# Optimization experiments

Measured on AMD Instinct MI355X. Metric: run time of the kernel, lower is better.

## Reference

```python
import jax, jax.numpy as jnp
import numpy as np

B, L, D_MODEL = 4, 2048, 1024
D_STATE, D_CONV, EXPAND, HEADDIM = 128, 4, 2, 64
D_INNER = EXPAND * D_MODEL            # 2048
NHEADS = D_INNER // HEADDIM           # 32
CONV_DIM = D_INNER + 2 * D_STATE      # 2304
D_IN_PROJ = 2 * D_INNER + 2 * D_STATE + NHEADS  # 4448
EPS = 1e-5


def _silu(v):
    return v * jax.nn.sigmoid(v)


def setup_inputs() -> dict:
    key = jax.random.key(0)
    ks = jax.random.split(key, 8)
    x = jax.random.normal(ks[0], (B, L, D_MODEL), dtype=jnp.float32)
    ln_w = jnp.ones((D_MODEL,), jnp.float32)
    ln_b = jnp.zeros((D_MODEL,), jnp.float32)
    in_proj_w = jax.random.normal(ks[1], (D_IN_PROJ, D_MODEL), jnp.float32) * 0.02
    conv_w = jax.random.normal(ks[2], (CONV_DIM, D_CONV), jnp.float32) * 0.2
    conv_b = jnp.zeros((CONV_DIM,), jnp.float32)
    # inverse-softplus of dt sampled in [1e-3, 1e-1], matching mamba2 dt init
    dt_bias = jnp.log(jnp.expm1(jax.random.uniform(ks[3], (NHEADS,), minval=0.001, maxval=0.1)))
    # A sampled uniform in [1,16], stored as log (A = -exp(A_log))
    A_log = jnp.log(jax.random.uniform(ks[4], (NHEADS,), minval=1.0, maxval=16.0))
    D = jnp.ones((NHEADS,), jnp.float32)
    rms_w = jnp.ones((D_INNER,), jnp.float32)
    out_proj_w = jax.random.normal(ks[5], (D_MODEL, D_INNER), jnp.float32) * 0.02
    return {"x": x, "ln_w": ln_w, "ln_b": ln_b, "in_proj_w": in_proj_w,
            "conv_w": conv_w, "conv_b": conv_b, "dt_bias": dt_bias,
            "A_log": A_log, "D": D, "rms_w": rms_w, "out_proj_w": out_proj_w}


def reference(x, ln_w, ln_b, in_proj_w, conv_w, conv_b, dt_bias, A_log, D, rms_w, out_proj_w):
    b = x.shape[0]
    # LayerNorm
    mu = x.mean(-1, keepdims=True)
    var = ((x - mu) ** 2).mean(-1, keepdims=True)
    u = (x - mu) * jax.lax.rsqrt(var + EPS) * ln_w + ln_b
    # input projection -> z | xBC | dt
    zxbcdt = jnp.einsum('bld,ed->ble', u, in_proj_w)
    z = zxbcdt[..., :D_INNER]
    xBC = zxbcdt[..., D_INNER:D_INNER + CONV_DIM]
    dt = jax.nn.softplus(zxbcdt[..., -NHEADS:] + dt_bias)  # (b,l,h)
    # causal depthwise conv along time (kernel D_CONV) + silu
    xpad = jnp.pad(xBC, ((0, 0), (D_CONV - 1, 0), (0, 0)))
    conv = conv_b + sum(conv_w[:, k] * xpad[:, k:k + L, :] for k in range(D_CONV))
    xBC = _silu(conv)
    xh = xBC[..., :D_INNER].reshape(b, L, NHEADS, HEADDIM)       # (b,l,h,p)
    Bm = xBC[..., D_INNER:D_INNER + D_STATE]                      # (b,l,n)
    Cm = xBC[..., D_INNER + D_STATE:]                             # (b,l,n)
    A = -jnp.exp(A_log)                                           # (h,)
    dA = jnp.exp(dt * A)                                          # (b,l,h)
    dtx = dt[..., None] * xh                                      # (b,l,h,p)

    def step(h, inp):
        dA_t, dtx_t, B_t, C_t = inp
        h = dA_t[:, :, None, None] * h + dtx_t[..., None] * B_t[:, None, None, :]
        y_t = jnp.einsum('bhpn,bn->bhp', h, C_t)
        return h, y_t

    h0 = jnp.zeros((b, NHEADS, HEADDIM, D_STATE), x.dtype)
    xs = (dA.transpose(1, 0, 2), dtx.transpose(1, 0, 2, 3),
          Bm.transpose(1, 0, 2), Cm.transpose(1, 0, 2))
    _, ys = jax.lax.scan(step, h0, xs)                            # (l,b,h,p)
    y = ys.transpose(1, 0, 2, 3) + D[None, None, :, None] * xh    # skip term
    y = y.reshape(b, L, D_INNER)
    # gated RMSNorm: rmsnorm(y * silu(z)) * weight
    g = y * _silu(z)
    g = g * jax.lax.rsqrt((g * g).mean(-1, keepdims=True) + EPS) * rms_w
    out = jnp.einsum('ble,de->bld', g, out_proj_w)
    # residual; dropout is identity in eval mode
    return out + x
```

## Files before the change

kernel.cpp:

```cpp
#include <hip/hip_runtime.h>
#include <hip/hip_bf16.h>

#define DEV __device__ __forceinline__

typedef unsigned short u16;
typedef unsigned int u32;
typedef float f32x4 __attribute__((ext_vector_type(4)));
typedef short s16x8 __attribute__((ext_vector_type(8)));

static constexpr int Bb = 4, Ll = 2048, DM = 1024, DI = 2048, NH = 32;
static constexpr int CD = 2304;
static constexpr int NP = 4384;
static constexpr int NP_PAD = 4480;
static constexpr int BL = Bb * Ll;
static constexpr int NC = 32;

DEV float u2f(u16 s) { return __uint_as_float(((u32)s) << 16); }
DEV u16 f2bu(float f) {
  __hip_bfloat16 h = __float2bfloat16(f);
  u16 s; __builtin_memcpy(&s, &h, 2); return s;
}
DEV float blo(u32 u) { return __uint_as_float(u << 16); }
DEV float bhi(u32 u) { return __uint_as_float(u & 0xffff0000u); }

DEV int swz64(int r, int k)  { return r * 64  + ((((k >> 3) ^ (r & 7))) << 3) + (k & 7); }

DEV void gl_lds16(const u16* g, u16* l) {
  __builtin_amdgcn_global_load_lds(
      (const __attribute__((address_space(1))) u32*)g,
      (__attribute__((address_space(3))) u32*)l, 16, 0, 0);
}

__global__ __launch_bounds__(256) void prep_kernel(const float* __restrict__ x,
    const float* __restrict__ w, const float* __restrict__ bia, u16* __restrict__ u,
    const float* __restrict__ w1, u16* __restrict__ W1b,
    const float* __restrict__ w2, u16* __restrict__ W2b) {
  __shared__ float rs[4], rs2[4];
  int tid = threadIdx.x;
  if (blockIdx.x < BL) {
    int row = blockIdx.x;
    const float4* xr = (const float4*)(x + (size_t)row * DM);
    float4 v = xr[tid];
    float s = v.x + v.y + v.z + v.w;
    float s2 = v.x*v.x + v.y*v.y + v.z*v.z + v.w*v.w;
    #pragma unroll
    for (int o = 32; o; o >>= 1) { s += __shfl_down(s, o); s2 += __shfl_down(s2, o); }
    int wv = tid >> 6, ln = tid & 63;
    if (ln == 0) { rs[wv] = s; rs2[wv] = s2; }
    __syncthreads();
    s = rs[0] + rs[1] + rs[2] + rs[3];
    s2 = rs2[0] + rs2[1] + rs2[2] + rs2[3];
    float mu = s * (1.f / DM);
    float var = s2 * (1.f / DM) - mu * mu;
    float inv = rsqrtf(var + 1e-5f);
    float4 wv4 = ((const float4*)w)[tid], bv4 = ((const float4*)bia)[tid];
    ushort4 o;
    o.x = f2bu((v.x - mu) * inv * wv4.x + bv4.x);
    o.y = f2bu((v.y - mu) * inv * wv4.y + bv4.y);
    o.z = f2bu((v.z - mu) * inv * wv4.z + bv4.z);
    o.w = f2bu((v.w - mu) * inv * wv4.w + bv4.w);
    ((ushort4*)(u + (size_t)row * DM))[tid] = o;
  } else {
    const int total1 = NP_PAD * 1024;
    int i = (blockIdx.x - BL) * 256 + tid;
    if (i < total1) {
      int r = i >> 10;
      W1b[i] = (r < NP) ? f2bu(w1[i]) : (u16)0;
    } else {
      int j = i - total1;
      if (j < 1024 * 2048) W2b[j] = f2bu(w2[j]);
    }
  }
}

template<int MODE>
__global__ __launch_bounds__(512, 4) void gemm2p(const u16* __restrict__ A,
    const u16* __restrict__ Bw, void* __restrict__ o0, u16* __restrict__ xbc,
    u16* __restrict__ dtraw, const float* __restrict__ resid) {
  constexpr int K = (MODE == 0) ? 1024 : 2048;
  constexpr int NT = K / 32;
  __shared__ u16 SH[24576];
  int tid = threadIdx.x, wid = tid >> 6, lane = tid & 63;
  int fr = lane & 15, fq = lane >> 4;
  int nb = blockIdx.x;
  int xcd = nb & 7, i = nb >> 3;
  int m0 = (xcd * 4 + (i & 3)) * 256;
  int n0 = (i >> 2) * 128;
  int wm = (wid >> 1) * 64, wn = (wid & 1) * 64;
  int ksrcE = (((lane & 3) ^ ((lane >> 3) & 3)) << 3);
  int lr = lane >> 2;

  f32x4 acc[4][4];
  #pragma unroll
  for (int a = 0; a < 4; a++)
    #pragma unroll
    for (int b = 0; b < 4; b++) acc[a][b] = (f32x4){0.f, 0.f, 0.f, 0.f};

  auto STGA = [&](int t, int dstE) {
    #pragma unroll
    for (int h = 0; h < 2; h++) {
      int r0 = h * 128 + wid * 16;
      gl_lds16(A + (size_t)(m0 + r0 + lr) * K + t * 32 + ksrcE, &SH[dstE + r0 * 32]);
    }
  };
  auto STGB = [&](int t, int dstE) {
    int r0 = wid * 16;
    gl_lds16(Bw + (size_t)(n0 + r0 + lr) * K + t * 32 + ksrcE, &SH[dstE + r0 * 32]);
  };

  STGA(0, 0);
  STGB(0, 16384);
  asm volatile("s_waitcnt vmcnt(0)\n\ts_barrier" ::: "memory");
  for (int t = 0; t < NT; t++) {
    int ca = (t & 1) * 8192, cbf = 16384 + (t & 1) * 4096;
    if (t < NT - 1) {
      STGA(t + 1, ((t + 1) & 1) * 8192);
      STGB(t + 1, 16384 + ((t + 1) & 1) * 4096);
      asm volatile("s_waitcnt vmcnt(3)\n\ts_barrier" ::: "memory");
    } else {
      asm volatile("s_waitcnt vmcnt(0)\n\ts_barrier" ::: "memory");
    }
    s16x8 bB[4];
    #pragma unroll
    for (int nf = 0; nf < 4; nf++) {
      int rb = wn + nf * 16 + fr;
      bB[nf] = *(const s16x8*)&SH[cbf + rb * 32 + ((fq ^ ((rb >> 1) & 3)) << 3)];
    }
    __builtin_amdgcn_s_setprio(1);
    #pragma unroll
    for (int mf = 0; mf < 4; mf++) {
      int ra = wm + mf * 16 + fr;
      s16x8 af = *(const s16x8*)&SH[ca + ra * 32 + ((fq ^ ((ra >> 1) & 3)) << 3)];
      #pragma unroll
      for (int nf = 0; nf < 4; nf++)
        acc[mf][nf] = __builtin_amdgcn_mfma_f32_16x16x32_bf16(af, bB[nf], acc[mf][nf], 0, 0, 0);
    }
    __builtin_amdgcn_s_setprio(0);
    asm volatile("s_barrier" ::: "memory");
  }
  if (MODE == 0) {
    u16* zbuf = (u16*)o0;
    #pragma unroll
    for (int mf = 0; mf < 4; mf++) {
      #pragma unroll
      for (int nf = 0; nf < 4; nf++) {
        int col = n0 + wn + nf * 16 + fr;
        #pragma unroll
        for (int r = 0; r < 4; r++) {
          int row = m0 + wm + mf * 16 + fq * 4 + r;
          float v = acc[mf][nf][r];
          if (col < 2048)       zbuf[(size_t)row * 2048 + col] = f2bu(v);
          else if (col < 4352)  xbc[(size_t)row * 2304 + (col - 2048)] = f2bu(v);
          else if (col < 4384)  dtraw[(size_t)row * 32 + (col - 4352)] = f2bu(v);
        }
      }
    }
  } else {
    float* of = (float*)o0;
    #pragma unroll
    for (int mf = 0; mf < 4; mf++) {
      #pragma unroll
      for (int nf = 0; nf < 4; nf++) {
        int col = n0 + wn + nf * 16 + fr;
        #pragma unroll
        for (int r = 0; r < 4; r++) {
          int row = m0 + wm + mf * 16 + fq * 4 + r;
          of[(size_t)row * 1024 + col] = acc[mf][nf][r] + resid[(size_t)row * 1024 + col];
        }
      }
    }
  }
}

__global__ __launch_bounds__(256) void convdt_kernel(const u16* __restrict__ xbc,
    const float* __restrict__ cw, const float* __restrict__ cb, u16* __restrict__ out,
    const u16* __restrict__ dtraw, const float* __restrict__ dtb,
    const float* __restrict__ alog, float* __restrict__ dtv, float* __restrict__ sv) {
  const int CONV_BLOCKS = (BL * (CD / 8)) / 256;
  if (blockIdx.x < CONV_BLOCKS) {
    int i = blockIdx.x * 256 + threadIdx.x;
    int c8 = i % (CD / 8);
    int bl = i / (CD / 8);
    int l = bl & (Ll - 1);
    int c0 = c8 * 8;
    uint4 R[4];
    #pragma unroll
    for (int k = 0; k < 4; k++) {
      int ls = l - 3 + k;
      if (ls >= 0) R[k] = *(const uint4*)(xbc + (size_t)(bl - 3 + k) * CD + c0);
      else         R[k] = (uint4){0u, 0u, 0u, 0u};
    }
    u16 o[8];
    #pragma unroll
    for (int e = 0; e < 8; e++) {
      float acc = cb[c0 + e];
      float4 wv = *(const float4*)(cw + (size_t)(c0 + e) * 4);
      float wk[4] = {wv.x, wv.y, wv.z, wv.w};
      #pragma unroll
      for (int k = 0; k < 4; k++) {
        u32 word = (&R[k].x)[e >> 1];
        float xv = (e & 1) ? bhi(word) : blo(word);
        acc += wk[k] * xv;
      }
      float sg = 1.f / (1.f + __expf(-acc));
      o[e] = f2bu(acc * sg);
    }
    uint4 ov;
    ov.x = (u32)o[0] | ((u32)o[1] << 16);
    ov.y = (u32)o[2] | ((u32)o[3] << 16);
    ov.z = (u32)o[4] | ((u32)o[5] << 16);
    ov.w = (u32)o[6] | ((u32)o[7] << 16);
    *(uint4*)(out + (size_t)bl * CD + c0) = ov;
  } else {
    int wid = threadIdx.x >> 6, lane = threadIdx.x & 63;
    int g = (blockIdx.x - CONV_BLOCKS) * 4 + wid;
    int b = g >> 10, h = (g >> 5) & 31, c = g & 31;
    int t = c * 64 + lane;
    float raw = u2f(dtraw[(size_t)(b * Ll + t) * 32 + h]);
    float v = raw + dtb[h];
    float dt = (v > 20.f) ? v : log1pf(__expf(v));
    float a = -dt * __expf(alog[h]);
    float s = a;
    #pragma unroll
    for (int o = 1; o < 64; o <<= 1) {
      float u = __shfl_up(s, o);
      if (lane >= o) s += u;
    }
    int idx = (b * 32 + h) * Ll + t;
    dtv[idx] = dt;
    sv[idx] = s;
  }
}

__global__ __launch_bounds__(256) void chunk_state(const u16* __restrict__ conv,
    const float* __restrict__ dtv, const float* __restrict__ sv,
    u16* __restrict__ S) {
  __shared__ u16 xsT[64 * 64];
  __shared__ u16 BT[128 * 64];
  int gid = blockIdx.x;
  int h = gid & 31, c = (gid >> 5) & 31, b = gid >> 10;
  int bh = b * 32 + h;
  int tid = threadIdx.x, w = tid >> 6, lane = tid & 63;
  int fr = lane & 15, fq = lane >> 4;
  int j = tid & 63, pg = tid >> 6;
  int tb = c * 64;
  const float* svb = sv + (size_t)bh * Ll + tb;
  const float* dvb = dtv + (size_t)bh * Ll + tb;
  const u16* cvb = conv + (size_t)(b * Ll + tb) * CD;
  float s_last = svb[63];
  float wj = __expf(s_last - svb[j]) * dvb[j];
  const u16* rowp = cvb + (size_t)j * CD;
  #pragma unroll
  for (int rep = 0; rep < 2; rep++) {
    int p0 = rep * 32 + pg * 8;
    uint4 v = *(const uint4*)(rowp + h * 64 + p0);
    u32 va[4] = {v.x, v.y, v.z, v.w};
    #pragma unroll
    for (int e = 0; e < 4; e++) {
      xsT[swz64(p0 + 2 * e, j)]     = f2bu(blo(va[e]) * wj);
      xsT[swz64(p0 + 2 * e + 1, j)] = f2bu(bhi(va[e]) * wj);
    }
  }
  #pragma unroll
  for (int rep = 0; rep < 4; rep++) {
    int n0 = rep * 32 + pg * 8;
    uint4 v = *(const uint4*)(rowp + DI + n0);
    u32 va[4] = {v.x, v.y, v.z, v.w};
    #pragma unroll
    for (int e = 0; e < 4; e++) {
      BT[swz64(n0 + 2 * e, j)]     = (u16)(va[e] & 0xffffu);
      BT[swz64(n0 + 2 * e + 1, j)] = (u16)(va[e] >> 16);
    }
  }
  __syncthreads();
  f32x4 acc[4][2];
  #pragma unroll
  for (int mi = 0; mi < 4; mi++)
    #pragma unroll
    for (int ni = 0; ni < 2; ni++) acc[mi][ni] = (f32x4){0.f, 0.f, 0.f, 0.f};
  #pragma unroll
  for (int ks = 0; ks < 2; ks++) {
    int k8 = ks * 4 + fq;
    s16x8 bfv[2];
    #pragma unroll
    for (int ni = 0; ni < 2; ni++) {
      int rb = w * 32 + ni * 16 + fr;
      bfv[ni] = *(const s16x8*)&BT[rb * 64 + ((k8 ^ (rb & 7)) << 3)];
    }
    #pragma unroll
    for (int mi = 0; mi < 4; mi++) {
      int ra = mi * 16 + fr;
      s16x8 af = *(const s16x8*)&xsT[ra * 64 + ((k8 ^ (ra & 7)) << 3)];
      #pragma unroll
      for (int ni = 0; ni < 2; ni++)
        acc[mi][ni] = __builtin_amdgcn_mfma_f32_16x16x32_bf16(af, bfv[ni], acc[mi][ni], 0, 0, 0);
    }
  }
  u16* Sc = S + ((size_t)bh * NC + c) * 8192;
  #pragma unroll
  for (int mi = 0; mi < 4; mi++) {
    #pragma unroll
    for (int ni = 0; ni < 2; ni++) {
      int p = mi * 16 + fq * 4;
      int n = w * 32 + ni * 16 + fr;
      #pragma unroll
      for (int r = 0; r < 4; r++)
        Sc[(size_t)(p + r) * 128 + n] = f2bu(acc[mi][ni][r]);
    }
  }
}

__global__ __launch_bounds__(256) void state_pass(u16* __restrict__ S,
    const float* __restrict__ sv) {
  int bh = blockIdx.x >> 2, q = blockIdx.x & 3;
  int o = q * 2048 + threadIdx.x * 8;
  const float* svb = sv + (size_t)bh * Ll;
  u16* base = S + (size_t)bh * NC * 8192 + o;
  float acc[8] = {0.f, 0.f, 0.f, 0.f, 0.f, 0.f, 0.f, 0.f};
  for (int c = 0; c < NC; c++) {
    uint4 sc = *(const uint4*)(base + (size_t)c * 8192);
    uint4 pre;
    pre.x = (u32)f2bu(acc[0]) | ((u32)f2bu(acc[1]) << 16);
    pre.y = (u32)f2bu(acc[2]) | ((u32)f2bu(acc[3]) << 16);
    pre.z = (u32)f2bu(acc[4]) | ((u32)f2bu(acc[5]) << 16);
    pre.w = (u32)f2bu(acc[6]) | ((u32)f2bu(acc[7]) << 16);
    *(uint4*)(base + (size_t)c * 8192) = pre;
    float E = __expf(svb[c * 64 + 63]);
    u32 wv[4] = {sc.x, sc.y, sc.z, sc.w};
    #pragma unroll
    for (int e = 0; e < 4; e++) {
      acc[2 * e]     = E * acc[2 * e]     + blo(wv[e]);
      acc[2 * e + 1] = E * acc[2 * e + 1] + bhi(wv[e]);
    }
  }
}

__global__ __launch_bounds__(256) void chunk_out(const u16* __restrict__ conv,
    const u16* __restrict__ hstart, const float* __restrict__ dtv,
    const float* __restrict__ sv, const float* __restrict__ Dp,
    u16* __restrict__ yb) {
  __shared__ u16 Ct[64 * 128];
  __shared__ u16 Bt[64 * 128];
  __shared__ u16 xT[64 * 64];
  __shared__ float svl[64], dtl[64], pexl[64];
  int gid = blockIdx.x;
  int h = gid & 31, c = (gid >> 5) & 31, b = gid >> 10;
  int tid = threadIdx.x, w = tid >> 6, lane = tid & 63;
  int fr = lane & 15, fq = lane >> 4;
  int tb = c * 64;
  const u16* cvb = conv + ((size_t)b * Ll + tb) * CD;
  const u16* hsrc = hstart + (((size_t)(b * 32 + h)) * NC + c) * 8192;
  int wp = w * 16, wj = w * 16;
  s16x8 h4[4];
  #pragma unroll
  for (int ks = 0; ks < 4; ks++) {
    int rb = wp + fr;
    int k8 = ks * 4 + fq;
    h4[ks] = *(const s16x8*)(hsrc + (size_t)rb * 128 + k8 * 8);
  }
  #pragma unroll
  for (int qq = 0; qq < 4; qq++) {
    int q = w * 4 + qq;
    int i = q * 4 + (lane >> 4);
    int s = lane & 15;
    int kc = ((s ^ (i & 7)) << 3);
    gl_lds16(cvb + (size_t)i * CD + 2176 + kc, &Ct[q * 512]);
    gl_lds16(cvb + (size_t)i * CD + 2048 + kc, &Bt[q * 512]);
  }
  {
    int j = tid & 63, pg = tid >> 6;
    const u16* rowp = cvb + (size_t)j * CD + h * 64;
    #pragma unroll
    for (int rep = 0; rep < 2; rep++) {
      int p0 = rep * 32 + pg * 8;
      uint4 v = *(const uint4*)(rowp + p0);
      u32 va[4] = {v.x, v.y, v.z, v.w};
      #pragma unroll
      for (int e = 0; e < 4; e++) {
        xT[swz64(p0 + 2 * e, j)]     = (u16)(va[e] & 0xffffu);
        xT[swz64(p0 + 2 * e + 1, j)] = (u16)(va[e] >> 16);
      }
    }
  }
  if (tid < 64) {
    float s = sv[(size_t)(b * 32 + h) * Ll + tb + tid];
    svl[tid] = s;
    pexl[tid] = __expf(s);
    dtl[tid] = dtv[(size_t)(b * 32 + h) * Ll + tb + tid];
  }
  __syncthreads();
  f32x4 g2[4];
  #pragma unroll
  for (int mi = 0; mi < 4; mi++) g2[mi] = (f32x4){0.f, 0.f, 0.f, 0.f};
  #pragma unroll
  for (int ks = 0; ks < 4; ks++) {
    int k8 = ks * 4 + fq;
    int rb = wj + fr;
    s16x8 bf = *(const s16x8*)&Bt[rb * 128 + ((k8 ^ (rb & 7)) << 3)];
    #pragma unroll
    for (int mi = 0; mi < 4; mi++) {
      int ra = mi * 16 + fr;
      s16x8 af = *(const s16x8*)&Ct[ra * 128 + ((k8 ^ (ra & 7)) << 3)];
      g2[mi] = __builtin_amdgcn_mfma_f32_16x16x32_bf16(af, bf, g2[mi], 0, 0, 0);
    }
  }
  u16 mv[4][4];
  #pragma unroll
  for (int mi = 0; mi < 4; mi++) {
    int jj = wj + fr;
    #pragma unroll
    for (int r = 0; r < 4; r++) {
      int ii = mi * 16 + fq * 4 + r;
      float v = 0.f;
      if (jj <= ii) v = g2[mi][r] * __expf(svl[ii] - svl[jj]) * dtl[jj];
      mv[mi][r] = f2bu(v);
    }
  }
  __syncthreads();
  #pragma unroll
  for (int mi = 0; mi < 4; mi++) {
    int jj = wj + fr;
    #pragma unroll
    for (int r = 0; r < 4; r++) {
      int ii = mi * 16 + fq * 4 + r;
      Bt[swz64(ii, jj)] = mv[mi][r];
    }
  }
  __syncthreads();
  f32x4 aY[4], a4[4];
  #pragma unroll
  for (int mi = 0; mi < 4; mi++) { aY[mi] = (f32x4){0.f, 0.f, 0.f, 0.f}; a4[mi] = (f32x4){0.f, 0.f, 0.f, 0.f}; }
  #pragma unroll
  for (int ks = 0; ks < 2; ks++) {
    int k8 = ks * 4 + fq;
    int rb = wp + fr;
    s16x8 bf = *(const s16x8*)&xT[rb * 64 + ((k8 ^ (rb & 7)) << 3)];
    #pragma unroll
    for (int mi = 0; mi < 4; mi++) {
      int ra = mi * 16 + fr;
      s16x8 af = *(const s16x8*)&Bt[ra * 64 + ((k8 ^ (ra & 7)) << 3)];
      aY[mi] = __builtin_amdgcn_mfma_f32_16x16x32_bf16(af, bf, aY[mi], 0, 0, 0);
    }
  }
  #pragma unroll
  for (int ks = 0; ks < 4; ks++) {
    int k8 = ks * 4 + fq;
    #pragma unroll
    for (int mi = 0; mi < 4; mi++) {
      int ra = mi * 16 + fr;
      s16x8 af = *(const s16x8*)&Ct[ra * 128 + ((k8 ^ (ra & 7)) << 3)];
      a4[mi] = __builtin_amdgcn_mfma_f32_16x16x32_bf16(af, h4[ks], a4[mi], 0, 0, 0);
    }
  }
  float Dh = Dp[h];
  u16* yrow = yb + ((size_t)b * Ll + tb) * DI + h * 64;
  #pragma unroll
  for (int mi = 0; mi < 4; mi++) {
    int p = wp + fr;
    #pragma unroll
    for (int r = 0; r < 4; r++) {
      int i = mi * 16 + fq * 4 + r;
      float xh = u2f(xT[swz64(p, i)]);
      yrow[(size_t)i * DI + p] = f2bu(aY[mi][r] + pexl[i] * a4[mi][r] + Dh * xh);
    }
  }
}

__global__ __launch_bounds__(256) void gate_rms(const u16* __restrict__ y,
    const u16* __restrict__ zbuf, const float* __restrict__ rw, u16* __restrict__ g) {
  int bl = blockIdx.x, tid = threadIdx.x;
  uint4 yv = ((const uint4*)(y + (size_t)bl * DI))[tid];
  uint4 zv = ((const uint4*)(zbuf + (size_t)bl * DI))[tid];
  u32 ya[4] = {yv.x, yv.y, yv.z, yv.w};
  u32 za[4] = {zv.x, zv.y, zv.z, zv.w};
  float gv[8];
  float ss = 0.f;
  #pragma unroll
  for (int jx = 0; jx < 4; jx++) {
    float y0 = blo(ya[jx]), y1 = bhi(ya[jx]);
    float z0 = blo(za[jx]), z1 = bhi(za[jx]);
    float s0 = z0 / (1.f + __expf(-z0));
    float s1 = z1 / (1.f + __expf(-z1));
    gv[jx * 2] = y0 * s0; gv[jx * 2 + 1] = y1 * s1;
    ss += gv[jx * 2] * gv[jx * 2] + gv[jx * 2 + 1] * gv[jx * 2 + 1];
  }
  #pragma unroll
  for (int o = 32; o; o >>= 1) ss += __shfl_down(ss, o);
  __shared__ float red[4];
  int wv = tid >> 6, ln = tid & 63;
  if (ln == 0) red[wv] = ss;
  __syncthreads();
  ss = red[0] + red[1] + red[2] + red[3];
  float scale = rsqrtf(ss * (1.f / DI) + 1e-5f);
  const float* rwp = rw + tid * 8;
  ushort4 o0, o1;
  o0.x = f2bu(gv[0] * scale * rwp[0]); o0.y = f2bu(gv[1] * scale * rwp[1]);
  o0.z = f2bu(gv[2] * scale * rwp[2]); o0.w = f2bu(gv[3] * scale * rwp[3]);
  o1.x = f2bu(gv[4] * scale * rwp[4]); o1.y = f2bu(gv[5] * scale * rwp[5]);
  o1.z = f2bu(gv[6] * scale * rwp[6]); o1.w = f2bu(gv[7] * scale * rwp[7]);
  ushort4* gp = (ushort4*)(g + (size_t)bl * DI + tid * 8);
  gp[0] = o0; gp[1] = o1;
}

extern "C" void kernel_launch(void* const* d_in, const int* in_sizes, int n_in,
                              void* d_out, int out_size, void* d_ws, size_t ws_size,
                              hipStream_t stream) {
  const float* x    = (const float*)d_in[0];
  const float* lnw  = (const float*)d_in[1];
  const float* lnb  = (const float*)d_in[2];
  const float* w1   = (const float*)d_in[3];
  const float* cw   = (const float*)d_in[4];
  const float* cb   = (const float*)d_in[5];
  const float* dtb  = (const float*)d_in[6];
  const float* alog = (const float*)d_in[7];
  const float* Dp   = (const float*)d_in[8];
  const float* rw   = (const float*)d_in[9];
  const float* w2   = (const float*)d_in[10];

  char* ws = (char*)d_ws;
  u16*   ub     = (u16*)(ws + 0);
  u16*   W1b    = (u16*)(ws + 16777216);
  u16*   conv   = (u16*)(ws + 0);
  u16*   zbuf   = (u16*)(ws + 37748736);
  u16*   xbc    = (u16*)(ws + 71303168);
  u16*   dtraw  = (u16*)(ws + 109051904);
  u16*   Sbuf   = (u16*)(ws + 71303168);
  u16*   gb     = (u16*)(ws + 71303168);
  float* dtv    = (float*)(ws + 138412032);
  float* sv     = (float*)(ws + 139460608);
  u16*   yb     = (u16*)(ws + 140509184);
  u16*   W2b    = (u16*)(ws + 174063616);
  if (ws_size < 178257920u) return;

  float* out = (float*)d_out;

  int cvt_blocks = (NP_PAD * 1024 + 1024 * 2048) / 256;
  prep_kernel<<<BL + cvt_blocks, 256, 0, stream>>>(x, lnw, lnb, ub, w1, W1b, w2, W2b);
  gemm2p<0><<<1120, 512, 0, stream>>>(ub, W1b, zbuf, xbc, dtraw, nullptr);
  convdt_kernel<<<(BL * (CD / 8)) / 256 + 1024, 256, 0, stream>>>(
      xbc, cw, cb, conv, dtraw, dtb, alog, dtv, sv);
  chunk_state<<<4096, 256, 0, stream>>>(conv, dtv, sv, Sbuf);
  state_pass<<<512, 256, 0, stream>>>(Sbuf, sv);
  chunk_out<<<4096, 256, 0, stream>>>(conv, Sbuf, dtv, sv, Dp, yb);
  gate_rms<<<BL, 256, 0, stream>>>(yb, zbuf, rw, gb);
  gemm2p<1><<<256, 512, 0, stream>>>(gb, W2b, out, nullptr, nullptr, x);
}
```

Before: 314.6 us.

## Fuse causal conv and dt/cumsum into chunk_state and chunk_out kernels

Removes the standalone convdt kernel. The depthwise conv+SiLU and the softplus dt plus wave prefix scan are now recomputed inside both chunk_state and chunk_out from the raw xbc and dtraw buffers. Per-chunk total decay is stored in a small Etot array for state_pass. This drops a full write and re-read of the conv output and dt/s arrays. In exchange the conv is computed twice with four-tap overlapping reads, and the B/C tiles in chunk_out lose their async global-to-LDS loads. The workspace layout is repacked.

```diff
diff --git a/kernel.cpp b/kernel.cpp
--- a/kernel.cpp
+++ b/kernel.cpp
@@ -29,6 +29,41 @@
   __builtin_amdgcn_global_load_lds(
       (const __attribute__((address_space(1))) u32*)g,
       (__attribute__((address_space(3))) u32*)l, 16, 0, 0);
+}
+
+DEV void conv8(const u16* __restrict__ xbcb, int pos, int col0,
+               const float* __restrict__ cw, const float* __restrict__ cb,
+               float* out) {
+  uint4 r[4];
+  #pragma unroll
+  for (int k = 0; k < 4; k++) {
+    int ls = pos - 3 + k;
+    if (ls >= 0) r[k] = *(const uint4*)(xbcb + (size_t)ls * CD + col0);
+    else         r[k] = (uint4){0u, 0u, 0u, 0u};
+  }
+  #pragma unroll
+  for (int e = 0; e < 8; e++) {
+    float acc = cb[col0 + e];
+    float4 wv = *(const float4*)(cw + (size_t)(col0 + e) * 4);
+    float wk[4] = {wv.x, wv.y, wv.z, wv.w};
+    #pragma unroll
+    for (int k = 0; k < 4; k++) {
+      u32 word = (&r[k].x)[e >> 1];
+      acc += wk[k] * ((e & 1) ? bhi(word) : blo(word));
+    }
+    float sg = 1.f / (1.f + __expf(-acc));
+    out[e] = acc * sg;
+  }
+}
+
+DEV float wave_scan(float a, int lane) {
+  float s = a;
+  #pragma unroll
+  for (int o = 1; o < 64; o <<= 1) {
+    float u = __shfl_up(s, o);
+    if (lane >= o) s += u;
+  }
+  return s;
 }
 
 __global__ __launch_bounds__(256) void prep_kernel(const float* __restrict__ x,
@@ -172,69 +207,10 @@
   }
 }
 
-__global__ __launch_bounds__(256) void convdt_kernel(const u16* __restrict__ xbc,
-    const float* __restrict__ cw, const float* __restrict__ cb, u16* __restrict__ out,
+__global__ __launch_bounds__(256) void chunk_state(const u16* __restrict__ xbc,
     const u16* __restrict__ dtraw, const float* __restrict__ dtb,
-    const float* __restrict__ alog, float* __restrict__ dtv, float* __restrict__ sv) {
-  const int CONV_BLOCKS = (BL * (CD / 8)) / 256;
-  if (blockIdx.x < CONV_BLOCKS) {
-    int i = blockIdx.x * 256 + threadIdx.x;
-    int c8 = i % (CD / 8);
-    int bl = i / (CD / 8);
-    int l = bl & (Ll - 1);
-    int c0 = c8 * 8;
-    uint4 R[4];
-    #pragma unroll
-    for (int k = 0; k < 4; k++) {
-      int ls = l - 3 + k;
-      if (ls >= 0) R[k] = *(const uint4*)(xbc + (size_t)(bl - 3 + k) * CD + c0);
-      else         R[k] = (uint4){0u, 0u, 0u, 0u};
-    }
-    u16 o[8];
-    #pragma unroll
-    for (int e = 0; e < 8; e++) {
-      float acc = cb[c0 + e];
-      float4 wv = *(const float4*)(cw + (size_t)(c0 + e) * 4);
-      float wk[4] = {wv.x, wv.y, wv.z, wv.w};
-      #pragma unroll
-      for (int k = 0; k < 4; k++) {
-        u32 word = (&R[k].x)[e >> 1];
-        float xv = (e & 1) ? bhi(word) : blo(word);
-        acc += wk[k] * xv;
-      }
-      float sg = 1.f / (1.f + __expf(-acc));
-      o[e] = f2bu(acc * sg);
-    }
-    uint4 ov;
-    ov.x = (u32)o[0] | ((u32)o[1] << 16);
-    ov.y = (u32)o[2] | ((u32)o[3] << 16);
-    ov.z = (u32)o[4] | ((u32)o[5] << 16);
-    ov.w = (u32)o[6] | ((u32)o[7] << 16);
-    *(uint4*)(out + (size_t)bl * CD + c0) = ov;
-  } else {
-    int wid = threadIdx.x >> 6, lane = threadIdx.x & 63;
-    int g = (blockIdx.x - CONV_BLOCKS) * 4 + wid;
-    int b = g >> 10, h = (g >> 5) & 31, c = g & 31;
-    int t = c * 64 + lane;
-    float raw = u2f(dtraw[(size_t)(b * Ll + t) * 32 + h]);
-    float v = raw + dtb[h];
-    float dt = (v > 20.f) ? v : log1pf(__expf(v));
-    float a = -dt * __expf(alog[h]);
-    float s = a;
-    #pragma unroll
-    for (int o = 1; o < 64; o <<= 1) {
-      float u = __shfl_up(s, o);
-      if (lane >= o) s += u;
-    }
-    int idx = (b * 32 + h) * Ll + t;
-    dtv[idx] = dt;
-    sv[idx] = s;
-  }
-}
-
-__global__ __launch_bounds__(256) void chunk_state(const u16* __restrict__ conv,
-    const float* __restrict__ dtv, const float* __restrict__ sv,
-    u16* __restrict__ S) {
+    const float* __restrict__ alog, const float* __restrict__ cw,
+    const float* __restrict__ cb, u16* __restrict__ S, float* __restrict__ Etot) {
   __shared__ u16 xsT[64 * 64];
   __shared__ u16 BT[128 * 64];
   int gid = blockIdx.x;
@@ -244,33 +220,29 @@
   int fr = lane & 15, fq = lane >> 4;
   int j = tid & 63, pg = tid >> 6;
   int tb = c * 64;
-  const float* svb = sv + (size_t)bh * Ll + tb;
-  const float* dvb = dtv + (size_t)bh * Ll + tb;
-  const u16* cvb = conv + (size_t)(b * Ll + tb) * CD;
-  float s_last = svb[63];
-  float wj = __expf(s_last - svb[j]) * dvb[j];
-  const u16* rowp = cvb + (size_t)j * CD;
+  const u16* xbcb = xbc + (size_t)b * Ll * CD;
+  float raw = u2f(dtraw[(size_t)(b * Ll + tb + j) * 32 + h]);
+  float v = raw + dtb[h];
+  float dt = (v > 20.f) ? v : log1pf(__expf(v));
+  float a = -dt * __expf(alog[h]);
+  float s = wave_scan(a, j);
+  float s_last = __shfl(s, 63);
+  float wj = __expf(s_last - s) * dt;
+  if (tid == 0) Etot[(size_t)bh * NC + c] = s_last;
+  float o8[8];
   #pragma unroll
   for (int rep = 0; rep < 2; rep++) {
     int p0 = rep * 32 + pg * 8;
-    uint4 v = *(const uint4*)(rowp + h * 64 + p0);
-    u32 va[4] = {v.x, v.y, v.z, v.w};
-    #pragma unroll
-    for (int e = 0; e < 4; e++) {
-      xsT[swz64(p0 + 2 * e, j)]     = f2bu(blo(va[e]) * wj);
-      xsT[swz64(p0 + 2 * e + 1, j)] = f2bu(bhi(va[e]) * wj);
-    }
+    conv8(xbcb, tb + j, h * 64 + p0, cw, cb, o8);
+    #pragma unroll
+    for (int m = 0; m < 8; m++) xsT[swz64(p0 + m, j)] = f2bu(o8[m] * wj);
   }
   #pragma unroll
   for (int rep = 0; rep < 4; rep++) {
     int n0 = rep * 32 + pg * 8;
-    uint4 v = *(const uint4*)(rowp + DI + n0);
-    u32 va[4] = {v.x, v.y, v.z, v.w};
-    #pragma unroll
-    for (int e = 0; e < 4; e++) {
-      BT[swz64(n0 + 2 * e, j)]     = (u16)(va[e] & 0xffffu);
-      BT[swz64(n0 + 2 * e + 1, j)] = (u16)(va[e] >> 16);
-    }
+    conv8(xbcb, tb + j, 2048 + n0, cw, cb, o8);
+    #pragma unroll
+    for (int m = 0; m < 8; m++) BT[swz64(n0 + m, j)] = f2bu(o8[m]);
   }
   __syncthreads();
   f32x4 acc[4][2];
@@ -311,10 +283,10 @@
 }
 
 __global__ __launch_bounds__(256) void state_pass(u16* __restrict__ S,
-    const float* __restrict__ sv) {
+    const float* __restrict__ Etot) {
   int bh = blockIdx.x >> 2, q = blockIdx.x & 3;
   int o = q * 2048 + threadIdx.x * 8;
-  const float* svb = sv + (size_t)bh * Ll;
+  const float* Eb = Etot + (size_t)bh * NC;
   u16* base = S + (size_t)bh * NC * 8192 + o;
   float acc[8] = {0.f, 0.f, 0.f, 0.f, 0.f, 0.f, 0.f, 0.f};
   for (int c = 0; c < NC; c++) {
@@ -325,7 +297,7 @@
     pre.z = (u32)f2bu(acc[4]) | ((u32)f2bu(acc[5]) << 16);
     pre.w = (u32)f2bu(acc[6]) | ((u32)f2bu(acc[7]) << 16);
     *(uint4*)(base + (size_t)c * 8192) = pre;
-    float E = __expf(svb[c * 64 + 63]);
+    float E = __expf(Eb[c]);
     u32 wv[4] = {sc.x, sc.y, sc.z, sc.w};
     #pragma unroll
     for (int e = 0; e < 4; e++) {
@@ -335,10 +307,11 @@
   }
 }
 
-__global__ __launch_bounds__(256) void chunk_out(const u16* __restrict__ conv,
-    const u16* __restrict__ hstart, const float* __restrict__ dtv,
-    const float* __restrict__ sv, const float* __restrict__ Dp,
-    u16* __restrict__ yb) {
+__global__ __launch_bounds__(256) void chunk_out(const u16* __restrict__ xbc,
+    const u16* __restrict__ dtraw, const u16* __restrict__ hstart,
+    const float* __restrict__ dtb, const float* __restrict__ alog,
+    const float* __restrict__ cw, const float* __restrict__ cb,
+    const float* __restrict__ Dp, u16* __restrict__ yb) {
   __shared__ u16 Ct[64 * 128];
   __shared__ u16 Bt[64 * 128];
   __shared__ u16 xT[64 * 64];
@@ -348,7 +321,7 @@
   int tid = threadIdx.x, w = tid >> 6, lane = tid & 63;
   int fr = lane & 15, fq = lane >> 4;
   int tb = c * 64;
-  const u16* cvb = conv + ((size_t)b * Ll + tb) * CD;
+  const u16* xbcb = xbc + (size_t)b * Ll * CD;
   const u16* hsrc = hstart + (((size_t)(b * 32 + h)) * NC + c) * 8192;
   int wp = w * 16, wj = w * 16;
   s16x8 h4[4];
@@ -358,35 +331,40 @@
     int k8 = ks * 4 + fq;
     h4[ks] = *(const s16x8*)(hsrc + (size_t)rb * 128 + k8 * 8);
   }
-  #pragma unroll
-  for (int qq = 0; qq < 4; qq++) {
-    int q = w * 4 + qq;
-    int i = q * 4 + (lane >> 4);
-    int s = lane & 15;
-    int kc = ((s ^ (i & 7)) << 3);
-    gl_lds16(cvb + (size_t)i * CD + 2176 + kc, &Ct[q * 512]);
-    gl_lds16(cvb + (size_t)i * CD + 2048 + kc, &Bt[q * 512]);
+  if (tid < 64) {
+    float raw = u2f(dtraw[(size_t)(b * Ll + tb + tid) * 32 + h]);
+    float v = raw + dtb[h];
+    float dt = (v > 20.f) ? v : log1pf(__expf(v));
+    float a = -dt * __expf(alog[h]);
+    float s = wave_scan(a, tid);
+    svl[tid] = s;
+    pexl[tid] = __expf(s);
+    dtl[tid] = dt;
   }
   {
     int j = tid & 63, pg = tid >> 6;
-    const u16* rowp = cvb + (size_t)j * CD + h * 64;
+    float o8[8];
+    u16 t8[8];
+    #pragma unroll
+    for (int rep = 0; rep < 4; rep++) {
+      int n0 = rep * 32 + pg * 8;
+      int kc = n0 >> 3;
+      conv8(xbcb, tb + j, 2048 + n0, cw, cb, o8);
+      #pragma unroll
+      for (int m = 0; m < 8; m++) t8[m] = f2bu(o8[m]);
+      *(uint4*)&Bt[j * 128 + ((kc ^ (j & 7)) << 3)] = *(const uint4*)t8;
+      conv8(xbcb, tb + j, 2176 + n0, cw, cb, o8);
+      #pragma unroll
+      for (int m = 0; m < 8; m++) t8[m] = f2bu(o8[m]);
+      *(uint4*)&Ct[j * 128 + ((kc ^ (j & 7)) << 3)] = *(const uint4*)t8;
+    }
     #pragma unroll
     for (int rep = 0; rep < 2; rep++) {
       int p0 = rep * 32 + pg * 8;
-      uint4 v = *(const uint4*)(rowp + p0);
-      u32 va[4] = {v.x, v.y, v.z, v.w};
-      #pragma unroll
-      for (int e = 0; e < 4; e++) {
-        xT[swz64(p0 + 2 * e, j)]     = (u16)(va[e] & 0xffffu);
-        xT[swz64(p0 + 2 * e + 1, j)] = (u16)(va[e] >> 16);
-      }
-    }
-  }
-  if (tid < 64) {
-    float s = sv[(size_t)(b * 32 + h) * Ll + tb + tid];
-    svl[tid] = s;
-    pexl[tid] = __expf(s);
-    dtl[tid] = dtv[(size_t)(b * 32 + h) * Ll + tb + tid];
+      conv8(xbcb, tb + j, h * 64 + p0, cw, cb, o8);
+      #pragma unroll
+      for (int m = 0; m < 8; m++) xT[swz64(p0 + m, j)] = f2bu(o8[m]);
+    }
   }
   __syncthreads();
   f32x4 g2[4];
@@ -520,28 +498,24 @@
   char* ws = (char*)d_ws;
   u16*   ub     = (u16*)(ws + 0);
   u16*   W1b    = (u16*)(ws + 16777216);
-  u16*   conv   = (u16*)(ws + 0);
-  u16*   zbuf   = (u16*)(ws + 37748736);
-  u16*   xbc    = (u16*)(ws + 71303168);
-  u16*   dtraw  = (u16*)(ws + 109051904);
-  u16*   Sbuf   = (u16*)(ws + 71303168);
-  u16*   gb     = (u16*)(ws + 71303168);
-  float* dtv    = (float*)(ws + 138412032);
-  float* sv     = (float*)(ws + 139460608);
-  u16*   yb     = (u16*)(ws + 140509184);
-  u16*   W2b    = (u16*)(ws + 174063616);
-  if (ws_size < 178257920u) return;
+  u16*   dtraw  = (u16*)(ws + 26214400);
+  u16*   zbuf   = (u16*)(ws + 27262976);
+  u16*   xbc    = (u16*)(ws + 60817408);
+  u16*   Sbuf   = (u16*)(ws + 98566144);
+  u16*   gb     = (u16*)(ws + 98566144);
+  u16*   yb     = (u16*)(ws + 165675008);
+  u16*   W2b    = (u16*)(ws + 199229440);
+  float* Etot   = (float*)(ws + 203423744);
+  if (ws_size < 203440128u) return;
 
   float* out = (float*)d_out;
 
   int cvt_blocks = (NP_PAD * 1024 + 1024 * 2048) / 256;
   prep_kernel<<<BL + cvt_blocks, 256, 0, stream>>>(x, lnw, lnb, ub, w1, W1b, w2, W2b);
   gemm2p<0><<<1120, 512, 0, stream>>>(ub, W1b, zbuf, xbc, dtraw, nullptr);
-  convdt_kernel<<<(BL * (CD / 8)) / 256 + 1024, 256, 0, stream>>>(
-      xbc, cw, cb, conv, dtraw, dtb, alog, dtv, sv);
-  chunk_state<<<4096, 256, 0, stream>>>(conv, dtv, sv, Sbuf);
-  state_pass<<<512, 256, 0, stream>>>(Sbuf, sv);
-  chunk_out<<<4096, 256, 0, stream>>>(conv, Sbuf, dtv, sv, Dp, yb);
+  chunk_state<<<4096, 256, 0, stream>>>(xbc, dtraw, dtb, alog, cw, cb, Sbuf, Etot);
+  state_pass<<<512, 256, 0, stream>>>(Sbuf, Etot);
+  chunk_out<<<4096, 256, 0, stream>>>(xbc, dtraw, Sbuf, dtb, alog, cw, cb, Dp, yb);
   gate_rms<<<BL, 256, 0, stream>>>(yb, zbuf, rw, gb);
   gemm2p<1><<<256, 512, 0, stream>>>(gb, W2b, out, nullptr, nullptr, x);
 }
```

Measured after the change: 434.5 us. +38.1%, slower.
